# Kernel optimization log

Measured on AMD Instinct MI355X. Metric: run time of the kernel, lower is better.

The kernel has to match this reference:

```python
import jax, jax.numpy as jnp
import numpy as np

B, S, D = 4, 128, 4096
H, KV, HD = 32, 8, 128
REP = H // KV  # GQA repeat factor = 4


def setup_inputs() -> dict:
    key = jax.random.key(0)
    ks = jax.random.split(key, 10)
    scale = 0.02
    x = jax.random.normal(ks[0], (B, S, D), dtype=jnp.float32)
    # projection weights stored as (in, out) so y = x @ W + b (== torch Linear)
    wq = jax.random.normal(ks[1], (D, H * HD), dtype=jnp.float32) * scale
    bq = jax.random.normal(ks[2], (H * HD,), dtype=jnp.float32) * scale
    wk = jax.random.normal(ks[3], (D, KV * HD), dtype=jnp.float32) * scale
    bk = jax.random.normal(ks[4], (KV * HD,), dtype=jnp.float32) * scale
    wv = jax.random.normal(ks[5], (D, KV * HD), dtype=jnp.float32) * scale
    bv = jax.random.normal(ks[6], (KV * HD,), dtype=jnp.float32) * scale
    wo = jax.random.normal(ks[7], (H * HD, D), dtype=jnp.float32) * scale
    bo = jax.random.normal(ks[8], (D,), dtype=jnp.float32) * scale
    # rotary frequencies: theta=10000, half-dim = HD//2 = 64
    inv_freq = 1.0 / (10000.0 ** (jnp.arange(0, HD, 2, dtype=jnp.float32) / HD))
    t = jnp.arange(S, dtype=jnp.float32)
    angles = jnp.outer(t, inv_freq)  # (S, 64)
    freqs_cos = jnp.cos(angles)
    freqs_sin = jnp.sin(angles)
    # additive causal mask (S, S): 0 on/below diagonal, -inf above
    mask = jnp.where(jnp.tril(jnp.ones((S, S), dtype=bool)), 0.0, -jnp.inf).astype(jnp.float32)
    cache_k = jnp.zeros((B, S, KV, HD), dtype=jnp.float32)
    cache_v = jnp.zeros((B, S, KV, HD), dtype=jnp.float32)
    return {
        "x": x, "start_pos": 0, "freqs_cos": freqs_cos, "freqs_sin": freqs_sin,
        "mask": mask, "cache_k": cache_k, "cache_v": cache_v,
        "wq": wq, "bq": bq, "wk": wk, "bk": bk, "wv": wv, "bv": bv,
        "wo": wo, "bo": bo,
    }


def _rope(t, cos, sin):
    # t: (B, S, h, HD); treat last dim as HD//2 complex pairs (real, imag)
    tr = t.reshape(*t.shape[:-1], HD // 2, 2)
    tre, tim = tr[..., 0], tr[..., 1]
    c = cos[None, :, None, :]  # (1, S, 1, HD//2)
    s = sin[None, :, None, :]
    out_re = tre * c - tim * s
    out_im = tre * s + tim * c
    return jnp.stack([out_re, out_im], axis=-1).reshape(t.shape)


def reference(x, start_pos, freqs_cos, freqs_sin, mask, cache_k, cache_v,
              wq, bq, wk, bk, wv, bv, wo, bo):
    bsz, seq_len, _ = x.shape
    q = (x @ wq + bq).reshape(bsz, seq_len, H, HD)
    k = (x @ wk + bk).reshape(bsz, seq_len, KV, HD)
    v = (x @ wv + bv).reshape(bsz, seq_len, KV, HD)
    q = _rope(q, freqs_cos, freqs_sin)
    k = _rope(k, freqs_cos, freqs_sin)
    # KV-cache append (functional)
    cache_k = cache_k.at[:bsz, start_pos:start_pos + seq_len].set(k)
    cache_v = cache_v.at[:bsz, start_pos:start_pos + seq_len].set(v)
    keys = cache_k[:bsz, :start_pos + seq_len]    # (B, T, KV, HD)
    vals = cache_v[:bsz, :start_pos + seq_len]
    # GQA head expansion (repeat_interleave on head dim)
    keys = jnp.repeat(keys, REP, axis=2)          # (B, T, H, HD)
    vals = jnp.repeat(vals, REP, axis=2)
    scale = 1.0 / jnp.sqrt(jnp.float32(HD))
    scores = jnp.einsum('bqhd,bkhd->bhqk', q, keys) * scale + mask
    attn = jax.nn.softmax(scores, axis=-1)
    out = jnp.einsum('bhqk,bkhd->bqhd', attn, vals).reshape(bsz, seq_len, H * HD)
    return out @ wo + bo
```

## Files before the change

### kernel.cpp

```cpp
#include <hip/hip_runtime.h>
#include <math.h>


#define B_   4
#define S_   128
#define D_   4096
#define H_   32
#define KV_  8
#define HD_  128
#define M_   (B_ * S_)
#define NQKV 6144
#define SCALE_ 0.088388347648318447f

typedef _Float16 half_t;
typedef half_t f16x8 __attribute__((ext_vector_type(8)));
typedef float  f32x4 __attribute__((ext_vector_type(4)));

__device__ inline void load_lds16(const void* g, void* l) {
    __builtin_amdgcn_global_load_lds((const __attribute__((address_space(1))) void*)g,
                                     (__attribute__((address_space(3))) void*)l,
                                     16, 0, 0);
}

__device__ void transpose_tile(const float* __restrict__ src, int Nsrc, int nsrc0,
                               int ndst0, int k0, int Ntot,
                               half_t* __restrict__ Wt, void* ldsraw) {
    float (*tile)[132] = (float(*)[132])ldsraw;
    const int t = threadIdx.x;
#pragma unroll
    for (int p = 0; p < 8; ++p) {
        int idx = t + p * 256;
        int r = idx >> 5, c4 = idx & 31;
        *(float4*)&tile[r][c4 * 4] =
            *(const float4*)&src[(size_t)(k0 + r) * Nsrc + nsrc0 + c4 * 4];
    }
    __syncthreads();
    const int n = t >> 1, kh = t & 1;
    __align__(16) half_t hs[32];
#pragma unroll
    for (int i = 0; i < 32; ++i)
        hs[i] = (half_t)tile[kh * 32 + i][n];
    size_t ob = ((size_t)(k0 >> 6) * Ntot + ndst0 + n) * 64 + kh * 32;
#pragma unroll
    for (int u = 0; u < 4; ++u)
        *(uint4*)&Wt[ob + u * 8] = *(uint4*)&hs[u * 8];
}

__global__ __launch_bounds__(256)
void prep_qkv(const float* __restrict__ wq, const float* __restrict__ wk,
              const float* __restrict__ wv, const float* __restrict__ x,
              half_t* __restrict__ Wt, half_t* __restrict__ x16) {
    __shared__ __align__(16) char lds[33792];
    const int bx = blockIdx.x;
    if (bx < 3072) {
        int nt = bx % 48, kt = bx / 48;
        const float* src; int Nsrc, ns0, nd0;
        if (nt < 32)      { src = wq; Nsrc = 4096; ns0 = nt * 128;        nd0 = nt * 128; }
        else if (nt < 40) { src = wk; Nsrc = 1024; ns0 = (nt - 32) * 128; nd0 = 4096 + (nt - 32) * 128; }
        else              { src = wv; Nsrc = 1024; ns0 = (nt - 40) * 128; nd0 = 5120 + (nt - 40) * 128; }
        transpose_tile(src, Nsrc, ns0, nd0, kt * 64, NQKV, Wt, lds);
    } else {
        int i0 = (bx - 3072) * 1024 + threadIdx.x;
#pragma unroll
        for (int j = 0; j < 4; ++j) {
            int i = i0 + j * 256;
            float4 f = ((const float4*)x)[i];
            __align__(8) half_t h4[4] = {(half_t)f.x, (half_t)f.y, (half_t)f.z, (half_t)f.w};
            ((uint2*)x16)[i] = *(uint2*)h4;
        }
    }
}

__global__ __launch_bounds__(512)
void gemm_qkv_fused(const half_t* __restrict__ x16, const half_t* __restrict__ Wt,
                    const float* __restrict__ bq, const float* __restrict__ bk,
                    const float* __restrict__ bv, const float* __restrict__ fc,
                    const float* __restrict__ fs, half_t* __restrict__ q16,
                    half_t* __restrict__ k16, half_t* __restrict__ vt16) {
    __shared__ __align__(16) char lds[67584];
    const int tid = threadIdx.x;
    const int nb = blockIdx.x % 48, mb = blockIdx.x / 48;
    const int m0 = mb * 128, n0 = nb * 128;
    const int g = tid >> 8;
    const int lane = tid & 63;
    const int quad = lane >> 4, l16 = lane & 15;
    const int w4 = (tid >> 6) & 3;
    const int wm = (w4 & 1) * 64, wn = (w4 >> 1) * 64;
    const int tB = tid & 192;

    half_t (*As)[64] = (half_t(*)[64])(lds + g * 32768);
    half_t (*Bs)[64] = (half_t(*)[64])(lds + g * 32768 + 16384);

    f32x4 acc[4][4] = {};
    const int kend = g * 2048 + 2048;
    for (int kc = g * 2048; kc < kend; kc += 64) {
        const half_t* Bslab = Wt + ((size_t)(kc >> 6) * NQKV + n0) * 64;
#pragma unroll
        for (int p = 0; p < 4; ++p) {
            int tb = p * 256 + tB;
            int task = tb + lane;
            int r = task >> 3;
            int os = (task ^ r) & 7;
            load_lds16(&x16[(size_t)(m0 + r) * 4096 + kc + os * 8], (half_t*)As + tb * 8);
            load_lds16(&Bslab[(size_t)r * 64 + os * 8],             (half_t*)Bs + tb * 8);
        }
        __syncthreads();
#pragma unroll
        for (int kk = 0; kk < 2; ++kk) {
            f16x8 af[4], bf[4];
#pragma unroll
            for (int i = 0; i < 4; ++i) {
                int ra = wm + i * 16 + l16;
                int rb = wn + i * 16 + l16;
                int L = kk * 4 + quad;
                af[i] = *(const f16x8*)&As[ra][(L ^ (ra & 7)) * 8];
                bf[i] = *(const f16x8*)&Bs[rb][(L ^ (rb & 7)) * 8];
            }
#pragma unroll
            for (int i = 0; i < 4; ++i)
#pragma unroll
                for (int j = 0; j < 4; ++j)
                    acc[i][j] = __builtin_amdgcn_mfma_f32_16x16x32_f16(af[i], bf[j], acc[i][j], 0, 0, 0);
        }
        __syncthreads();
    }

    float (*Tf)[132] = (float(*)[132])lds;
    if (g == 1) {
#pragma unroll
        for (int i = 0; i < 4; ++i)
#pragma unroll
            for (int j = 0; j < 4; ++j)
#pragma unroll
                for (int rg = 0; rg < 4; ++rg)
                    Tf[wm + i * 16 + quad * 4 + rg][wn + j * 16 + l16] = acc[i][j][rg];
    }
    __syncthreads();
    if (g == 0) {
#pragma unroll
        for (int i = 0; i < 4; ++i)
#pragma unroll
            for (int j = 0; j < 4; ++j)
#pragma unroll
                for (int rg = 0; rg < 4; ++rg)
                    acc[i][j][rg] += Tf[wm + i * 16 + quad * 4 + rg][wn + j * 16 + l16];
    }

    if (n0 < 5120) {
        if (g == 0) {
            const bool isQ = n0 < 4096;
            const float* bias = isQ ? bq : bk;
            const int bOff = isQ ? 0 : 4096;
            half_t* dst = isQ ? q16 : k16;
            const int ldd = isQ ? 4096 : 1024;
#pragma unroll
            for (int i = 0; i < 4; ++i)
#pragma unroll
                for (int j = 0; j < 4; ++j) {
                    const int col = n0 + wn + j * 16 + l16;
                    const int d2 = (col >> 1) & 63;
                    const float bcol = bias[col - bOff];
#pragma unroll
                    for (int rg = 0; rg < 4; ++rg) {
                        const int row = m0 + wm + i * 16 + quad * 4 + rg;
                        float v = acc[i][j][rg] + bcol;
                        float o = __shfl_xor(v, 1);
                        const int iloc = row & 127;
                        const float c = fc[iloc * 64 + d2], sn = fs[iloc * 64 + d2];
                        float ov = (l16 & 1) ? (o * sn + v * c)
                                             : (v * c - o * sn);
                        float o2 = __shfl_xor(ov, 1);
                        if (!(l16 & 1)) {
                            __align__(4) half_t hh[2] = {(half_t)ov, (half_t)o2};
                            *(unsigned int*)&dst[(size_t)row * ldd + (col - bOff)] =
                                *(unsigned int*)hh;
                        }
                    }
                }
        }
    } else {
        __syncthreads();
        half_t (*Th)[136] = (half_t(*)[136])lds;
        if (g == 0) {
#pragma unroll
            for (int i = 0; i < 4; ++i)
#pragma unroll
                for (int j = 0; j < 4; ++j) {
                    const int cl = wn + j * 16 + l16;
                    const float bcol = bv[n0 - 5120 + cl];
#pragma unroll
                    for (int rg = 0; rg < 4; ++rg)
                        Th[wm + i * 16 + quad * 4 + rg][cl] = (half_t)(acc[i][j][rg] + bcol);
                }
        }
        __syncthreads();
        const int d = tid >> 2, iq = tid & 3;
        const int kv = (n0 - 5120) >> 7;
        __align__(16) half_t hs[32];
#pragma unroll
        for (int u = 0; u < 32; ++u) hs[u] = Th[iq * 32 + u][d];
        size_t base = ((size_t)(mb * 8 + kv) * 128 + d) * 128 + iq * 32;
#pragma unroll
        for (int u = 0; u < 4; ++u)
            *(uint4*)&vt16[base + u * 8] = *(uint4*)&hs[u * 8];
    }
}

__global__ __launch_bounds__(256, 2)
void attn_wo(const half_t* __restrict__ q16, const half_t* __restrict__ k16,
             const half_t* __restrict__ vt16, half_t* __restrict__ a16,
             const float* __restrict__ wo, half_t* __restrict__ WtO) {
    __shared__ __align__(16) char lds[62464];
    if (blockIdx.x >= 512) {
        int t = blockIdx.x - 512;
        transpose_tile(wo, 4096, (t & 31) * 128, (t & 31) * 128, (t >> 5) * 64,
                       4096, WtO, lds);
        return;
    }
    half_t (*Qs)[136] = (half_t(*)[136])lds;
    half_t (*Ks)[136] = (half_t(*)[136])(lds + 8704);
    float (*Ps)[132]  = (float(*)[132])(lds + 43520);
    float (*red)[16]  = (float(*)[16])(lds + 60416);

    const int tid = threadIdx.x;
    const int qi = blockIdx.x & 3, h = (blockIdx.x >> 2) & 31, b = blockIdx.x >> 7;
    const int kv = h >> 2;
    const int qbase = qi * 32;
    const int lane = tid & 63, w = tid >> 6;
    const int quad = lane >> 4, l16 = lane & 15;
    const int m0 = (w & 1) * 16, half64 = (w >> 1) * 64;

#pragma unroll
    for (int p = 0; p < 2; ++p) {
        int task = tid + p * 256;
        int r = task >> 4, c = task & 15;
        *(uint4*)&Qs[r][c * 8] =
            *(const uint4*)&q16[((size_t)(b * 128 + qbase + r) * 32 + h) * 128 + c * 8];
    }
#pragma unroll
    for (int p = 0; p < 8; ++p) {
        int task = tid + p * 256;
        int r = task >> 4, c = task & 15;
        *(uint4*)&Ks[r][c * 8] =
            *(const uint4*)&k16[((size_t)(b * 128 + r) * 8 + kv) * 128 + c * 8];
    }
    __syncthreads();

    f32x4 s[4] = {};
#pragma unroll
    for (int kc = 0; kc < 4; ++kc) {
        f16x8 af = *(const f16x8*)&Qs[m0 + l16][kc * 32 + quad * 8];
#pragma unroll
        for (int jb = 0; jb < 4; ++jb) {
            f16x8 bf = *(const f16x8*)&Ks[half64 + jb * 16 + l16][kc * 32 + quad * 8];
            s[jb] = __builtin_amdgcn_mfma_f32_16x16x32_f16(af, bf, s[jb], 0, 0, 0);
        }
    }
#pragma unroll
    for (int jb = 0; jb < 4; ++jb) {
        int j = half64 + jb * 16 + l16;
#pragma unroll
        for (int rg = 0; rg < 4; ++rg) {
            int row = m0 + quad * 4 + rg;
            Ps[row][j] = (j <= qbase + row) ? s[jb][rg] * SCALE_ : -1e30f;
        }
    }
    __syncthreads();

    const int r = tid >> 3, seg = tid & 7;
    float mx = -1e30f;
#pragma unroll
    for (int i = 0; i < 16; ++i) mx = fmaxf(mx, Ps[r][seg * 16 + i]);
    red[r][seg] = mx;
    __syncthreads();

    uint4 vstage[8];
#pragma unroll
    for (int p = 0; p < 8; ++p) {
        int task = tid + p * 256;
        int rr = task >> 4, c = task & 15;
        vstage[p] = *(const uint4*)&vt16[((size_t)(b * 8 + kv) * 128 + rr) * 128 + c * 8];
    }
    float m = red[r][0];
#pragma unroll
    for (int i = 1; i < 8; ++i) m = fmaxf(m, red[r][i]);
    float sum = 0.f;
#pragma unroll
    for (int i = 0; i < 16; ++i) {
        float e = __expf(Ps[r][seg * 16 + i] - m);
        Ps[r][seg * 16 + i] = e;
        sum += e;
    }
    red[r][8 + seg] = sum;
#pragma unroll
    for (int p = 0; p < 8; ++p) {
        int task = tid + p * 256;
        int rr = task >> 4, c = task & 15;
        *(uint4*)&Ks[rr][c * 8] = vstage[p];
    }
    __syncthreads();

    float tot = 0.f;
#pragma unroll
    for (int i = 0; i < 8; ++i) tot += red[r][8 + i];
    float inv = 1.0f / tot;
#pragma unroll
    for (int i = 0; i < 16; ++i)
        Qs[r][seg * 16 + i] = (half_t)(Ps[r][seg * 16 + i] * inv);
    __syncthreads();

    f32x4 o[4] = {};
#pragma unroll
    for (int jc = 0; jc < 4; ++jc) {
        f16x8 af = *(const f16x8*)&Qs[m0 + l16][jc * 32 + quad * 8];
#pragma unroll
        for (int db = 0; db < 4; ++db) {
            f16x8 bf = *(const f16x8*)&Ks[half64 + db * 16 + l16][jc * 32 + quad * 8];
            o[db] = __builtin_amdgcn_mfma_f32_16x16x32_f16(af, bf, o[db], 0, 0, 0);
        }
    }
#pragma unroll
    for (int db = 0; db < 4; ++db) {
        int d = half64 + db * 16 + l16;
#pragma unroll
        for (int rg = 0; rg < 4; ++rg) {
            int row = m0 + quad * 4 + rg;
            a16[(size_t)(b * 128 + qbase + row) * 4096 + h * 128 + d] = (half_t)o[db][rg];
        }
    }
}

__global__ __launch_bounds__(512)
void gemm_o_fused(const half_t* __restrict__ a16, const half_t* __restrict__ WtO,
                  const float* __restrict__ bo, float* __restrict__ out) {
    __shared__ __align__(16) char lds[49152];
    const int tid = threadIdx.x;
    const int nb = blockIdx.x & 31, mb = blockIdx.x >> 5;
    const int m0 = mb * 64, n0 = nb * 128;
    const int g = tid >> 8;
    const int lane = tid & 63;
    const int quad = lane >> 4, l16 = lane & 15;
    const int w4 = (tid >> 6) & 3;
    const int wn = w4 * 32;
    const int tB = tid & 192;

    half_t (*As)[64] = (half_t(*)[64])(lds + g * 24576);
    half_t (*Bs)[64] = (half_t(*)[64])(lds + g * 24576 + 8192);

    f32x4 acc[4][2] = {};
    const int kend = g * 2048 + 2048;
    for (int kc = g * 2048; kc < kend; kc += 64) {
        const half_t* Bslab = WtO + ((size_t)(kc >> 6) * 4096 + n0) * 64;
#pragma unroll
        for (int p = 0; p < 4; ++p) {
            int tb = p * 256 + tB;
            int task = tb + lane;
            int r = task >> 3;
            int os = (task ^ r) & 7;
            load_lds16(&Bslab[(size_t)r * 64 + os * 8], (half_t*)Bs + tb * 8);
            if (p < 2)
                load_lds16(&a16[(size_t)(m0 + r) * 4096 + kc + os * 8], (half_t*)As + tb * 8);
        }
        __syncthreads();
#pragma unroll
        for (int kk = 0; kk < 2; ++kk) {
            f16x8 af[4], bf[2];
#pragma unroll
            for (int i = 0; i < 4; ++i) {
                int ra = i * 16 + l16;
                af[i] = *(const f16x8*)&As[ra][((kk * 4 + quad) ^ (ra & 7)) * 8];
            }
#pragma unroll
            for (int j = 0; j < 2; ++j) {
                int rb = wn + j * 16 + l16;
                bf[j] = *(const f16x8*)&Bs[rb][((kk * 4 + quad) ^ (rb & 7)) * 8];
            }
#pragma unroll
            for (int i = 0; i < 4; ++i)
#pragma unroll
                for (int j = 0; j < 2; ++j)
                    acc[i][j] = __builtin_amdgcn_mfma_f32_16x16x32_f16(af[i], bf[j], acc[i][j], 0, 0, 0);
        }
        __syncthreads();
    }

    float (*Tf)[132] = (float(*)[132])lds;
    if (g == 1) {
#pragma unroll
        for (int i = 0; i < 4; ++i)
#pragma unroll
            for (int j = 0; j < 2; ++j)
#pragma unroll
                for (int rg = 0; rg < 4; ++rg)
                    Tf[i * 16 + quad * 4 + rg][wn + j * 16 + l16] = acc[i][j][rg];
    }
    __syncthreads();
    if (g == 0) {
#pragma unroll
        for (int i = 0; i < 4; ++i)
#pragma unroll
            for (int j = 0; j < 2; ++j) {
                const int col = n0 + wn + j * 16 + l16;
                const float bcol = bo[col];
#pragma unroll
                for (int rg = 0; rg < 4; ++rg) {
                    const int row = m0 + i * 16 + quad * 4 + rg;
                    out[(size_t)row * 4096 + col] =
                        acc[i][j][rg] + Tf[i * 16 + quad * 4 + rg][wn + j * 16 + l16] + bcol;
                }
            }
    }
}

extern "C" void kernel_launch(void* const* d_in, const int* in_sizes, int n_in,
                              void* d_out, int out_size, void* d_ws, size_t ws_size,
                              hipStream_t stream) {
    const float* x    = (const float*)d_in[0];
    const float* fc   = (const float*)d_in[2];
    const float* fs   = (const float*)d_in[3];
    const float* wq   = (const float*)d_in[7];
    const float* bq   = (const float*)d_in[8];
    const float* wk   = (const float*)d_in[9];
    const float* bk   = (const float*)d_in[10];
    const float* wv   = (const float*)d_in[11];
    const float* bv   = (const float*)d_in[12];
    const float* wo   = (const float*)d_in[13];
    const float* bo   = (const float*)d_in[14];
    float* out = (float*)d_out;

    half_t* x16  = (half_t*)d_ws;
    half_t* a16  = x16 + 2097152;
    half_t* q16  = a16 + 2097152;
    half_t* k16  = q16 + 2097152;
    half_t* vt16 = k16 + 524288;
    half_t* Wt   = vt16 + 524288;
    half_t* WtO  = Wt;

    prep_qkv<<<3584, 256, 0, stream>>>(wq, wk, wv, x, Wt, x16);

    gemm_qkv_fused<<<192, 512, 0, stream>>>(x16, Wt, bq, bk, bv, fc, fs,
                                            q16, k16, vt16);

    attn_wo<<<2560, 256, 0, stream>>>(q16, k16, vt16, a16, wo, WtO);

    gemm_o_fused<<<256, 512, 0, stream>>>(a16, WtO, bo, out);
}
```

Measured before the change: 314.5 us.

## Replace split-K GEMMs with double-buffered 64x128 tiles and swizzled block order

Both projection GEMMs drop the intra-block split-K scheme, where two 256-thread groups each covered half of K and reduced their partials through LDS. They now use a shared double-buffered 64x128 tile routine that issues the next K-slab's LDS loads while the current one is being computed. The QKV GEMM moves from 128-row tiles to 64-row tiles with 256 threads, doubling its grid to 384 blocks. Both kernels remap block indices so consecutive blocks share weight columns, which should improve L2 reuse. The aim is to remove the reduction and serialized load-then-compute stalls, at the cost of less per-block reuse of A and B tiles and a different V-transpose epilogue indexing.

Measured after the change: 301.5 us. -4.1%, faster.

```diff
diff --git a/kernel.cpp b/kernel.cpp
--- a/kernel.cpp
+++ b/kernel.cpp
@@ -71,135 +71,149 @@
     }
 }
 
-__global__ __launch_bounds__(512)
+__device__ __forceinline__ void stage64x128(const half_t* __restrict__ A,
+                                            const half_t* __restrict__ Bbase,
+                                            int N, int m0, int n0, int kc,
+                                            half_t* AsD, half_t* BsD, int tid) {
+    const int lane = tid & 63, tB = tid & 192;
+    const half_t* Bslab = Bbase + ((size_t)(kc >> 6) * N + n0) * 64;
+#pragma unroll
+    for (int p = 0; p < 2; ++p) {
+        int tb = p * 256 + tB;
+        int task = tb + lane;
+        int r = task >> 3, os = (task ^ r) & 7;
+        load_lds16(&A[(size_t)(m0 + r) * 4096 + kc + os * 8], AsD + tb * 8);
+    }
+#pragma unroll
+    for (int p = 0; p < 4; ++p) {
+        int tb = p * 256 + tB;
+        int task = tb + lane;
+        int r = task >> 3, os = (task ^ r) & 7;
+        load_lds16(&Bslab[(size_t)r * 64 + os * 8], BsD + tb * 8);
+    }
+}
+
+__device__ __forceinline__ void compute64x128(const half_t* AsD, const half_t* BsD,
+                                              int tid, f32x4 (&acc)[4][2]) {
+    const int lane = tid & 63;
+    const int quad = lane >> 4, l16 = lane & 15;
+    const int wn = (tid >> 6) * 32;
+    half_t (*As)[64] = (half_t(*)[64])AsD;
+    half_t (*Bs)[64] = (half_t(*)[64])BsD;
+#pragma unroll
+    for (int kk = 0; kk < 2; ++kk) {
+        f16x8 af[4], bf[2];
+        int L = kk * 4 + quad;
+#pragma unroll
+        for (int i = 0; i < 4; ++i) {
+            int ra = i * 16 + l16;
+            af[i] = *(const f16x8*)&As[ra][(L ^ (ra & 7)) * 8];
+        }
+#pragma unroll
+        for (int j = 0; j < 2; ++j) {
+            int rb = wn + j * 16 + l16;
+            bf[j] = *(const f16x8*)&Bs[rb][(L ^ (rb & 7)) * 8];
+        }
+#pragma unroll
+        for (int i = 0; i < 4; ++i)
+#pragma unroll
+            for (int j = 0; j < 2; ++j)
+                acc[i][j] = __builtin_amdgcn_mfma_f32_16x16x32_f16(af[i], bf[j], acc[i][j], 0, 0, 0);
+    }
+}
+
+__device__ __forceinline__ void gemm64x128(const half_t* __restrict__ A,
+                                           const half_t* __restrict__ Bbase,
+                                           int N, int m0, int n0, char* lds,
+                                           f32x4 (&acc)[4][2]) {
+    const int tid = threadIdx.x;
+    half_t* As0 = (half_t*)lds;
+    half_t* Bs0 = (half_t*)(lds + 16384);
+    stage64x128(A, Bbase, N, m0, n0, 0, As0, Bs0, tid);
+    __syncthreads();
+    int cur = 0;
+    for (int it = 0; it < 63; ++it) {
+        int nxt = cur ^ 1;
+        stage64x128(A, Bbase, N, m0, n0, (it + 1) * 64,
+                    As0 + nxt * 4096, Bs0 + nxt * 8192, tid);
+        compute64x128(As0 + cur * 4096, Bs0 + cur * 8192, tid, acc);
+        __syncthreads();
+        cur = nxt;
+    }
+    compute64x128(As0 + cur * 4096, Bs0 + cur * 8192, tid, acc);
+    __syncthreads();
+}
+
+__global__ __launch_bounds__(256, 2)
 void gemm_qkv_fused(const half_t* __restrict__ x16, const half_t* __restrict__ Wt,
                     const float* __restrict__ bq, const float* __restrict__ bk,
                     const float* __restrict__ bv, const float* __restrict__ fc,
                     const float* __restrict__ fs, half_t* __restrict__ q16,
                     half_t* __restrict__ k16, half_t* __restrict__ vt16) {
-    __shared__ __align__(16) char lds[67584];
+    __shared__ __align__(16) char lds[49152];
+    const int bx = blockIdx.x;
+    const int o = (bx & 7) * 48 + (bx >> 3);
+    const int nb = o >> 3, mb = o & 7;
+    const int m0 = mb * 64, n0 = nb * 128;
+
+    f32x4 acc[4][2] = {};
+    gemm64x128(x16, Wt, NQKV, m0, n0, lds, acc);
+
     const int tid = threadIdx.x;
-    const int nb = blockIdx.x % 48, mb = blockIdx.x / 48;
-    const int m0 = mb * 128, n0 = nb * 128;
-    const int g = tid >> 8;
     const int lane = tid & 63;
     const int quad = lane >> 4, l16 = lane & 15;
-    const int w4 = (tid >> 6) & 3;
-    const int wm = (w4 & 1) * 64, wn = (w4 >> 1) * 64;
-    const int tB = tid & 192;
-
-    half_t (*As)[64] = (half_t(*)[64])(lds + g * 32768);
-    half_t (*Bs)[64] = (half_t(*)[64])(lds + g * 32768 + 16384);
-
-    f32x4 acc[4][4] = {};
-    const int kend = g * 2048 + 2048;
-    for (int kc = g * 2048; kc < kend; kc += 64) {
-        const half_t* Bslab = Wt + ((size_t)(kc >> 6) * NQKV + n0) * 64;
-#pragma unroll
-        for (int p = 0; p < 4; ++p) {
-            int tb = p * 256 + tB;
-            int task = tb + lane;
-            int r = task >> 3;
-            int os = (task ^ r) & 7;
-            load_lds16(&x16[(size_t)(m0 + r) * 4096 + kc + os * 8], (half_t*)As + tb * 8);
-            load_lds16(&Bslab[(size_t)r * 64 + os * 8],             (half_t*)Bs + tb * 8);
-        }
-        __syncthreads();
-#pragma unroll
-        for (int kk = 0; kk < 2; ++kk) {
-            f16x8 af[4], bf[4];
-#pragma unroll
-            for (int i = 0; i < 4; ++i) {
-                int ra = wm + i * 16 + l16;
-                int rb = wn + i * 16 + l16;
-                int L = kk * 4 + quad;
-                af[i] = *(const f16x8*)&As[ra][(L ^ (ra & 7)) * 8];
-                bf[i] = *(const f16x8*)&Bs[rb][(L ^ (rb & 7)) * 8];
-            }
-#pragma unroll
-            for (int i = 0; i < 4; ++i)
-#pragma unroll
-                for (int j = 0; j < 4; ++j)
-                    acc[i][j] = __builtin_amdgcn_mfma_f32_16x16x32_f16(af[i], bf[j], acc[i][j], 0, 0, 0);
-        }
-        __syncthreads();
-    }
-
-    float (*Tf)[132] = (float(*)[132])lds;
-    if (g == 1) {
+    const int wn = (tid >> 6) * 32;
+
+    if (n0 < 5120) {
+        const bool isQ = n0 < 4096;
+        const float* bias = isQ ? bq : bk;
+        const int bOff = isQ ? 0 : 4096;
+        half_t* dst = isQ ? q16 : k16;
+        const int ldd = isQ ? 4096 : 1024;
 #pragma unroll
         for (int i = 0; i < 4; ++i)
 #pragma unroll
-            for (int j = 0; j < 4; ++j)
-#pragma unroll
-                for (int rg = 0; rg < 4; ++rg)
-                    Tf[wm + i * 16 + quad * 4 + rg][wn + j * 16 + l16] = acc[i][j][rg];
-    }
-    __syncthreads();
-    if (g == 0) {
-#pragma unroll
-        for (int i = 0; i < 4; ++i)
-#pragma unroll
-            for (int j = 0; j < 4; ++j)
-#pragma unroll
-                for (int rg = 0; rg < 4; ++rg)
-                    acc[i][j][rg] += Tf[wm + i * 16 + quad * 4 + rg][wn + j * 16 + l16];
-    }
-
-    if (n0 < 5120) {
-        if (g == 0) {
-            const bool isQ = n0 < 4096;
-            const float* bias = isQ ? bq : bk;
-            const int bOff = isQ ? 0 : 4096;
-            half_t* dst = isQ ? q16 : k16;
-            const int ldd = isQ ? 4096 : 1024;
-#pragma unroll
-            for (int i = 0; i < 4; ++i)
-#pragma unroll
-                for (int j = 0; j < 4; ++j) {
-                    const int col = n0 + wn + j * 16 + l16;
-                    const int d2 = (col >> 1) & 63;
-                    const float bcol = bias[col - bOff];
-#pragma unroll
-                    for (int rg = 0; rg < 4; ++rg) {
-                        const int row = m0 + wm + i * 16 + quad * 4 + rg;
-                        float v = acc[i][j][rg] + bcol;
-                        float o = __shfl_xor(v, 1);
-                        const int iloc = row & 127;
-                        const float c = fc[iloc * 64 + d2], sn = fs[iloc * 64 + d2];
-                        float ov = (l16 & 1) ? (o * sn + v * c)
-                                             : (v * c - o * sn);
-                        float o2 = __shfl_xor(ov, 1);
-                        if (!(l16 & 1)) {
-                            __align__(4) half_t hh[2] = {(half_t)ov, (half_t)o2};
-                            *(unsigned int*)&dst[(size_t)row * ldd + (col - bOff)] =
-                                *(unsigned int*)hh;
-                        }
+            for (int j = 0; j < 2; ++j) {
+                const int col = n0 + wn + j * 16 + l16;
+                const int d2 = (col >> 1) & 63;
+                const float bcol = bias[col - bOff];
+#pragma unroll
+                for (int rg = 0; rg < 4; ++rg) {
+                    const int row = m0 + i * 16 + quad * 4 + rg;
+                    float v = acc[i][j][rg] + bcol;
+                    float p = __shfl_xor(v, 1);
+                    const int iloc = row & 127;
+                    const float c = fc[iloc * 64 + d2], sn = fs[iloc * 64 + d2];
+                    float ov = (l16 & 1) ? (p * sn + v * c)
+                                         : (v * c - p * sn);
+                    float o2 = __shfl_xor(ov, 1);
+                    if (!(l16 & 1)) {
+                        __align__(4) half_t hh[2] = {(half_t)ov, (half_t)o2};
+                        *(unsigned int*)&dst[(size_t)row * ldd + (col - bOff)] =
+                            *(unsigned int*)hh;
                     }
                 }
-        }
+            }
     } else {
+        half_t (*Th)[136] = (half_t(*)[136])lds;
+#pragma unroll
+        for (int i = 0; i < 4; ++i)
+#pragma unroll
+            for (int j = 0; j < 2; ++j) {
+                const int cl = wn + j * 16 + l16;
+                const float bcol = bv[n0 - 5120 + cl];
+#pragma unroll
+                for (int rg = 0; rg < 4; ++rg)
+                    Th[i * 16 + quad * 4 + rg][cl] = (half_t)(acc[i][j][rg] + bcol);
+            }
         __syncthreads();
-        half_t (*Th)[136] = (half_t(*)[136])lds;
-        if (g == 0) {
-#pragma unroll
-            for (int i = 0; i < 4; ++i)
-#pragma unroll
-                for (int j = 0; j < 4; ++j) {
-                    const int cl = wn + j * 16 + l16;
-                    const float bcol = bv[n0 - 5120 + cl];
-#pragma unroll
-                    for (int rg = 0; rg < 4; ++rg)
-                        Th[wm + i * 16 + quad * 4 + rg][cl] = (half_t)(acc[i][j][rg] + bcol);
-                }
-        }
-        __syncthreads();
-        const int d = tid >> 2, iq = tid & 3;
+        const int d = tid >> 1, ih = tid & 1;
         const int kv = (n0 - 5120) >> 7;
+        const int b = mb >> 1, i0 = (mb & 1) * 64;
         __align__(16) half_t hs[32];
 #pragma unroll
-        for (int u = 0; u < 32; ++u) hs[u] = Th[iq * 32 + u][d];
-        size_t base = ((size_t)(mb * 8 + kv) * 128 + d) * 128 + iq * 32;
+        for (int u = 0; u < 32; ++u) hs[u] = Th[ih * 32 + u][d];
+        size_t base = ((size_t)(b * 8 + kv) * 128 + d) * 128 + i0 + ih * 32;
 #pragma unroll
         for (int u = 0; u < 4; ++u)
             *(uint4*)&vt16[base + u * 8] = *(uint4*)&hs[u * 8];
@@ -330,86 +344,34 @@
     }
 }
 
-__global__ __launch_bounds__(512)
+__global__ __launch_bounds__(256, 2)
 void gemm_o_fused(const half_t* __restrict__ a16, const half_t* __restrict__ WtO,
                   const float* __restrict__ bo, float* __restrict__ out) {
     __shared__ __align__(16) char lds[49152];
+    const int bx = blockIdx.x;
+    const int o = (bx & 7) * 32 + (bx >> 3);
+    const int nb = o >> 3, mb = o & 7;
+    const int m0 = mb * 64, n0 = nb * 128;
+
+    f32x4 acc[4][2] = {};
+    gemm64x128(a16, WtO, 4096, m0, n0, lds, acc);
+
     const int tid = threadIdx.x;
-    const int nb = blockIdx.x & 31, mb = blockIdx.x >> 5;
-    const int m0 = mb * 64, n0 = nb * 128;
-    const int g = tid >> 8;
     const int lane = tid & 63;
     const int quad = lane >> 4, l16 = lane & 15;
-    const int w4 = (tid >> 6) & 3;
-    const int wn = w4 * 32;
-    const int tB = tid & 192;
-
-    half_t (*As)[64] = (half_t(*)[64])(lds + g * 24576);
-    half_t (*Bs)[64] = (half_t(*)[64])(lds + g * 24576 + 8192);
-
-    f32x4 acc[4][2] = {};
-    const int kend = g * 2048 + 2048;
-    for (int kc = g * 2048; kc < kend; kc += 64) {
-        const half_t* Bslab = WtO + ((size_t)(kc >> 6) * 4096 + n0) * 64;
-#pragma unroll
-        for (int p = 0; p < 4; ++p) {
-            int tb = p * 256 + tB;
-            int task = tb + lane;
-            int r = task >> 3;
-            int os = (task ^ r) & 7;
-            load_lds16(&Bslab[(size_t)r * 64 + os * 8], (half_t*)Bs + tb * 8);
-            if (p < 2)
-                load_lds16(&a16[(size_t)(m0 + r) * 4096 + kc + os * 8], (half_t*)As + tb * 8);
-        }
-        __syncthreads();
-#pragma unroll
-        for (int kk = 0; kk < 2; ++kk) {
-            f16x8 af[4], bf[2];
-#pragma unroll
-            for (int i = 0; i < 4; ++i) {
-                int ra = i * 16 + l16;
-                af[i] = *(const f16x8*)&As[ra][((kk * 4 + quad) ^ (ra & 7)) * 8];
+    const int wn = (tid >> 6) * 32;
+#pragma unroll
+    for (int i = 0; i < 4; ++i)
+#pragma unroll
+        for (int j = 0; j < 2; ++j) {
+            const int col = n0 + wn + j * 16 + l16;
+            const float bcol = bo[col];
+#pragma unroll
+            for (int rg = 0; rg < 4; ++rg) {
+                const int row = m0 + i * 16 + quad * 4 + rg;
+                out[(size_t)row * 4096 + col] = acc[i][j][rg] + bcol;
             }
-#pragma unroll
-            for (int j = 0; j < 2; ++j) {
-                int rb = wn + j * 16 + l16;
-                bf[j] = *(const f16x8*)&Bs[rb][((kk * 4 + quad) ^ (rb & 7)) * 8];
-            }
-#pragma unroll
-            for (int i = 0; i < 4; ++i)
-#pragma unroll
-                for (int j = 0; j < 2; ++j)
-                    acc[i][j] = __builtin_amdgcn_mfma_f32_16x16x32_f16(af[i], bf[j], acc[i][j], 0, 0, 0);
-        }
-        __syncthreads();
-    }
-
-    float (*Tf)[132] = (float(*)[132])lds;
-    if (g == 1) {
-#pragma unroll
-        for (int i = 0; i < 4; ++i)
-#pragma unroll
-            for (int j = 0; j < 2; ++j)
-#pragma unroll
-                for (int rg = 0; rg < 4; ++rg)
-                    Tf[i * 16 + quad * 4 + rg][wn + j * 16 + l16] = acc[i][j][rg];
-    }
-    __syncthreads();
-    if (g == 0) {
-#pragma unroll
-        for (int i = 0; i < 4; ++i)
-#pragma unroll
-            for (int j = 0; j < 2; ++j) {
-                const int col = n0 + wn + j * 16 + l16;
-                const float bcol = bo[col];
-#pragma unroll
-                for (int rg = 0; rg < 4; ++rg) {
-                    const int row = m0 + i * 16 + quad * 4 + rg;
-                    out[(size_t)row * 4096 + col] =
-                        acc[i][j][rg] + Tf[i * 16 + quad * 4 + rg][wn + j * 16 + l16] + bcol;
-                }
-            }
-    }
+        }
 }
 
 extern "C" void kernel_launch(void* const* d_in, const int* in_sizes, int n_in,
@@ -438,10 +400,10 @@
 
     prep_qkv<<<3584, 256, 0, stream>>>(wq, wk, wv, x, Wt, x16);
 
-    gemm_qkv_fused<<<192, 512, 0, stream>>>(x16, Wt, bq, bk, bv, fc, fs,
+    gemm_qkv_fused<<<384, 256, 0, stream>>>(x16, Wt, bq, bk, bv, fc, fs,
                                             q16, k16, vt16);
 
     attn_wo<<<2560, 256, 0, stream>>>(q16, k16, vt16, a16, wo, WtO);
 
-    gemm_o_fused<<<256, 512, 0, stream>>>(a16, WtO, bo, out);
-}
+    gemm_o_fused<<<256, 256, 0, stream>>>(a16, WtO, bo, out);
+}
```
